# Kernel optimization log

Hardware: AMD Instinct MI355X
Metric: run time of the kernel (lower is better)

Reference implementation:

```python
import jax, jax.numpy as jnp
import numpy as np

G, C, L, D, H, NCLS = 64, 32, 128, 64, 128, 10


def setup_inputs() -> dict:
    key = jax.random.key(0)
    ks = jax.random.split(key, 5)
    scale = 0.05
    return {
        "cycle_reps": jax.random.normal(ks[0], (G, C, L, D), dtype=jnp.float32),
        "W_ih": jax.random.normal(ks[1], (4 * H, D), dtype=jnp.float32) * scale,
        "W_hh": jax.random.normal(ks[2], (4 * H, H), dtype=jnp.float32) * scale,
        "b_ih": jnp.zeros((4 * H,), dtype=jnp.float32),
        "b_hh": jnp.zeros((4 * H,), dtype=jnp.float32),
        "W_cls": jax.random.normal(ks[3], (NCLS, H), dtype=jnp.float32) * scale,
        "b_cls": jnp.zeros((NCLS,), dtype=jnp.float32),
    }


def _lstm_seq_sum(x, W_ih, W_hh, b):
    """Run a single-layer LSTM over x [B, L, D]; return sum of hidden states over L -> [B, H]."""
    B = x.shape[0]
    Hh = W_hh.shape[1]
    # precompute input-side gate pre-activations for all timesteps: [L, B, 4H]
    xg = jnp.einsum('bld,gd->lbg', x, W_ih) + b

    def step(carry, xg_t):
        h, c = carry
        gates = xg_t + h @ W_hh.T  # [B, 4H]
        i, f, g, o = jnp.split(gates, 4, axis=-1)  # torch i/f/g/o gate order
        i = jax.nn.sigmoid(i)
        f = jax.nn.sigmoid(f)
        g = jnp.tanh(g)
        o = jax.nn.sigmoid(o)
        c = f * c + i * g
        h = o * jnp.tanh(c)
        return (h, c), h

    init = (jnp.zeros((B, Hh), x.dtype), jnp.zeros((B, Hh), x.dtype))
    _, hs = jax.lax.scan(step, init, xg)  # hs: [L, B, H]
    return hs.sum(axis=0)


def reference(cycle_reps, W_ih, W_hh, b_ih, b_hh, W_cls, b_cls):
    Gn, Cn, Ln, Dn = cycle_reps.shape
    x = cycle_reps.reshape(Gn * Cn, Ln, Dn)
    rep = _lstm_seq_sum(x, W_ih, W_hh, b_ih + b_hh)  # [G*C, H]: sum of LSTM outputs over seq
    rep = rep.reshape(Gn, Cn, -1)
    # torch.var_mean over the cycle axis; only the mean is used as the graph rep
    graph_mean = rep.mean(axis=1)  # [G, H]
    logits = graph_mean @ W_cls.T + b_cls  # classifier_gnn
    return jax.nn.log_softmax(logits, axis=1)
```

## Files before the change

kernel.cpp:

```cpp
#include <hip/hip_runtime.h>
#include <hip/hip_bf16.h>

#define NSEQ 2048
#define LSEQ 128
#define DIN  64
#define HID  128
#define NCLS 10
#define XPAD 72
#define CHK  16

typedef __attribute__((ext_vector_type(8))) short bfrag8;
typedef __attribute__((ext_vector_type(4))) float facc4;

__device__ __forceinline__ short f2bf(float f) {
    union { __hip_bfloat16 b; short s; } u;
    u.b = __float2bfloat16(f);
    return u.s;
}

__device__ __forceinline__ bfrag8 load_bf16_frag(const float* __restrict__ p) {
    bfrag8 r;
#pragma unroll
    for (int j = 0; j < 8; ++j) r[j] = f2bf(p[j]);
    return r;
}

__device__ __forceinline__ float fast_sigmoid(float x) {
    float e = __builtin_amdgcn_exp2f(-1.4426950408889634f * x);
    return __builtin_amdgcn_rcpf(1.0f + e);
}
__device__ __forceinline__ float fast_tanh(float x) {
    float e = __builtin_amdgcn_exp2f(2.8853900817779268f * x);
    return 1.0f - 2.0f * __builtin_amdgcn_rcpf(1.0f + e);
}

__global__ __launch_bounds__(512) void lstm_fused(
    const float* __restrict__ x,
    const float* __restrict__ Wih,
    const float* __restrict__ Whh,
    const float* __restrict__ bih,
    const float* __restrict__ bhh,
    float* __restrict__ rep)
{
    __shared__ __align__(16) __hip_bfloat16 hbuf[2][16][136];
    __shared__ __align__(16) __hip_bfloat16 xs[2][CHK][8][XPAD];

    const int tid  = threadIdx.x;
    const int w    = tid >> 6;
    const int lane = tid & 63;
    const int ln   = lane & 15;
    const int qd   = lane >> 4;
    const int s0   = blockIdx.x * 8;
    const int khid = w * 16 + ln;
    const int sq0  = (qd & 1) * 4 + (qd >> 1) * 2;
    const int sq1  = sq0 + 1;
    const bool hi  = (qd >= 2);

    bfrag8 whh[4][4];
    bfrag8 wih[4][2];
    float  biasv[4];
#pragma unroll
    for (int g = 0; g < 4; ++g) {
        const int col = g * HID + khid;
        biasv[g] = bih[col] + bhh[col];
#pragma unroll
        for (int k0 = 0; k0 < 4; ++k0)
            whh[g][k0] = load_bf16_frag(Whh + col * HID + k0 * 32 + qd * 8);
#pragma unroll
        for (int k0 = 0; k0 < 2; ++k0)
            wih[g][k0] = load_bf16_frag(Wih + col * DIN + k0 * 32 + qd * 8);
    }

    {
        unsigned int* p = (unsigned int*)&hbuf[0][0][0];
        for (int i = tid; i < 2 * 16 * 136 / 2; i += 512) p[i] = 0u;
    }

    const float* xsrc = x + (size_t)(s0 + w) * (LSEQ * DIN) + lane * 16;
    const int stt = lane >> 2;
    const int sdd = (lane & 3) * 16;

    {
        float4 a0 = ((const float4*)xsrc)[0];
        float4 a1 = ((const float4*)xsrc)[1];
        float4 a2 = ((const float4*)xsrc)[2];
        float4 a3 = ((const float4*)xsrc)[3];
        bfrag8 o0, o1;
#pragma unroll
        for (int j = 0; j < 4; ++j) { o0[j] = f2bf(((float*)&a0)[j]); o0[4+j] = f2bf(((float*)&a1)[j]); }
#pragma unroll
        for (int j = 0; j < 4; ++j) { o1[j] = f2bf(((float*)&a2)[j]); o1[4+j] = f2bf(((float*)&a3)[j]); }
        *(bfrag8*)&xs[0][stt][w][sdd]     = o0;
        *(bfrag8*)&xs[0][stt][w][sdd + 8] = o1;
    }

    float cst[2]  = {0.f, 0.f};
    float hsum[2] = {0.f, 0.f};

    __syncthreads();

    facc4 accA[4], accB[4];
    {
        bfrag8 x0 = *(const bfrag8*)(&xs[0][0][ln & 7][qd * 8]);
        bfrag8 x1 = *(const bfrag8*)(&xs[0][0][ln & 7][32 + qd * 8]);
#pragma unroll
        for (int g = 0; g < 4; ++g) {
            accA[g] = (facc4){biasv[g], biasv[g], biasv[g], biasv[g]};
            accA[g] = __builtin_amdgcn_mfma_f32_16x16x32_bf16(x0, wih[g][0], accA[g], 0, 0, 0);
            accA[g] = __builtin_amdgcn_mfma_f32_16x16x32_bf16(x1, wih[g][1], accA[g], 0, 0, 0);
        }
    }

    int cur = 0;

#define STEP(ACCIN, ACCOUT, CT)                                                          \
    {                                                                                    \
        const int ct = (CT);                                                             \
                                             \
        bfrag8 hf[4];                                                                    \
        _Pragma("unroll")                                                                \
        for (int k0 = 0; k0 < 4; ++k0)                                                   \
            hf[k0] = *(const bfrag8*)(&hbuf[cur][ln][k0 * 32 + qd * 8]);                 \
             \
        const int nbuf = (ct < CHK - 1) ? buf : (buf ^ 1);                               \
        const int nct  = (ct + 1) & (CHK - 1);                                           \
        bfrag8 xf0 = *(const bfrag8*)(&xs[nbuf][nct][ln & 7][qd * 8]);                   \
        bfrag8 xf1 = *(const bfrag8*)(&xs[nbuf][nct][ln & 7][32 + qd * 8]);              \
                    \
        _Pragma("unroll")                                                                \
        for (int g = 0; g < 4; ++g)                                                      \
            _Pragma("unroll")                                                            \
            for (int k0 = 0; k0 < 4; ++k0)                                               \
                ACCIN[g] = __builtin_amdgcn_mfma_f32_16x16x32_bf16(hf[k0], whh[g][k0], ACCIN[g], 0, 0, 0); \
                \
        float rc2[4], rc3[4];                                                            \
        _Pragma("unroll")                                                                \
        for (int g = 0; g < 4; ++g) {                                                    \
            rc2[g] = __shfl_xor(ACCIN[g][2], 32);                                        \
            rc3[g] = __shfl_xor(ACCIN[g][3], 32);                                        \
        }                                                                                \
                              \
        _Pragma("unroll")                                                                \
        for (int g = 0; g < 4; ++g) {                                                    \
            ACCOUT[g] = (facc4){biasv[g], biasv[g], biasv[g], biasv[g]};                 \
            ACCOUT[g] = __builtin_amdgcn_mfma_f32_16x16x32_bf16(xf0, wih[g][0], ACCOUT[g], 0, 0, 0); \
            ACCOUT[g] = __builtin_amdgcn_mfma_f32_16x16x32_bf16(xf1, wih[g][1], ACCOUT[g], 0, 0, 0); \
        }                                                                                \
        if (ct == 0 && more) {                      \
            const float* p = xsrc + (chunk + 1) * (CHK * DIN);                           \
            l0 = ((const float4*)p)[0];                                                  \
            l1 = ((const float4*)p)[1];                                                  \
            l2 = ((const float4*)p)[2];                                                  \
            l3 = ((const float4*)p)[3];                                                  \
        }                                                                                \
        if (ct == 12 && more) {                   \
            bfrag8 o0, o1;                                                               \
            _Pragma("unroll")                                                            \
            for (int j = 0; j < 4; ++j) { o0[j] = f2bf(((float*)&l0)[j]); o0[4+j] = f2bf(((float*)&l1)[j]); } \
            _Pragma("unroll")                                                            \
            for (int j = 0; j < 4; ++j) { o1[j] = f2bf(((float*)&l2)[j]); o1[4+j] = f2bf(((float*)&l3)[j]); } \
            *(bfrag8*)&xs[buf ^ 1][stt][w][sdd]     = o0;                                \
            *(bfrag8*)&xs[buf ^ 1][stt][w][sdd + 8] = o1;                                \
        }                                                                                \
                               \
        short hb[2];                                                                     \
        _Pragma("unroll")                                                                \
        for (int j = 0; j < 2; ++j) {                                                    \
            float u0 = hi ? (j ? rc3[0] : rc2[0]) : ACCIN[0][j];                         \
            float u1 = hi ? (j ? rc3[1] : rc2[1]) : ACCIN[1][j];                         \
            float u2 = hi ? (j ? rc3[2] : rc2[2]) : ACCIN[2][j];                         \
            float u3 = hi ? (j ? rc3[3] : rc2[3]) : ACCIN[3][j];                         \
            float iv = fast_sigmoid(u0);                                                 \
            float fv = fast_sigmoid(u1);                                                 \
            float gv = fast_tanh(u2);                                                    \
            float ov = fast_sigmoid(u3);                                                 \
            float c  = fv * cst[j] + iv * gv;                                            \
            cst[j]   = c;                                                                \
            float hv = ov * fast_tanh(c);                                                \
            hsum[j] += hv;                                                               \
            hb[j]    = f2bf(hv);                                                         \
        }                                                                                \
        ((short*)&hbuf[cur ^ 1][sq0][0])[khid] = hb[0];                                  \
        ((short*)&hbuf[cur ^ 1][sq1][0])[khid] = hb[1];                                  \
        __syncthreads();                                                                 \
        cur ^= 1;                                                                        \
    }

    for (int chunk = 0; chunk < LSEQ / CHK; ++chunk) {
        const int buf = chunk & 1;
        const bool more = chunk < (LSEQ / CHK - 1);
        float4 l0, l1, l2, l3;
#pragma unroll 1
        for (int ct2 = 0; ct2 < CHK / 2; ++ct2) {
            STEP(accA, accB, 2 * ct2);
            STEP(accB, accA, 2 * ct2 + 1);
        }
    }
#undef STEP

    rep[(size_t)(s0 + sq0) * HID + khid] = hsum[0];
    rep[(size_t)(s0 + sq1) * HID + khid] = hsum[1];
}

__global__ __launch_bounds__(128) void cls_kernel(
    const float* __restrict__ rep,
    const float* __restrict__ Wcls,
    const float* __restrict__ bcls,
    float* __restrict__ out)
{
    __shared__ float m_s[HID];
    __shared__ float logits_s[NCLS];
    const int g = blockIdx.x;
    const int h = threadIdx.x;

    float s = 0.f;
#pragma unroll 4
    for (int c = 0; c < 32; ++c)
        s += rep[((size_t)g * 32 + c) * HID + h];
    m_s[h] = s * (1.0f / 32.0f);
    __syncthreads();

    if (h < NCLS) {
        float acc = bcls[h];
        for (int k = 0; k < HID; ++k)
            acc += m_s[k] * Wcls[h * HID + k];
        logits_s[h] = acc;
    }
    __syncthreads();

    if (h < NCLS) {
        float mx = logits_s[0];
#pragma unroll
        for (int j = 1; j < NCLS; ++j) mx = fmaxf(mx, logits_s[j]);
        float se = 0.f;
#pragma unroll
        for (int j = 0; j < NCLS; ++j)
            se += __builtin_amdgcn_exp2f((logits_s[j] - mx) * 1.4426950408889634f);
        float lse = mx + 0.6931471805599453f * __builtin_amdgcn_logf(se);
        out[g * NCLS + h] = logits_s[h] - lse;
    }
}

extern "C" void kernel_launch(void* const* d_in, const int* in_sizes, int n_in,
                              void* d_out, int out_size, void* d_ws, size_t ws_size,
                              hipStream_t stream) {
    const float* x    = (const float*)d_in[0];
    const float* Wih  = (const float*)d_in[1];
    const float* Whh  = (const float*)d_in[2];
    const float* bih  = (const float*)d_in[3];
    const float* bhh  = (const float*)d_in[4];
    const float* Wcls = (const float*)d_in[5];
    const float* bcls = (const float*)d_in[6];

    float* rep = (float*)d_ws;

    lstm_fused<<<NSEQ / 8, 512, 0, stream>>>(x, Wih, Whh, bih, bhh, rep);
    cls_kernel<<<64, 128, 0, stream>>>(rep, Wcls, bcls, (float*)d_out);
}
```

Measured before the change: 201.3 us.

## Fuse classifier into LSTM kernel via atomic ticket, switch to fp16 MFMA

The classifier kernel is removed. Each LSTM block atomically adds its per-graph hidden-state mean into a workspace buffer, and the last block, found through an atomic ticket counter, computes logits and log-softmax. Weights, inputs and hidden state switch from bf16 to fp16 MFMA, and the cross-half lane shuffle uses permlane32_swap where available. This saves one kernel launch and the rep round-trip, and it adds a memset, float atomics and a serialized tail in the last block.

```diff
diff --git a/kernel.cpp b/kernel.cpp
--- a/kernel.cpp
+++ b/kernel.cpp
@@ -9,19 +9,14 @@
 #define XPAD 72
 #define CHK  16
 
-typedef __attribute__((ext_vector_type(8))) short bfrag8;
-typedef __attribute__((ext_vector_type(4))) float facc4;
-
-__device__ __forceinline__ short f2bf(float f) {
-    union { __hip_bfloat16 b; short s; } u;
-    u.b = __float2bfloat16(f);
-    return u.s;
-}
-
-__device__ __forceinline__ bfrag8 load_bf16_frag(const float* __restrict__ p) {
-    bfrag8 r;
-#pragma unroll
-    for (int j = 0; j < 8; ++j) r[j] = f2bf(p[j]);
+typedef _Float16 f16x8 __attribute__((ext_vector_type(8)));
+typedef float    facc4 __attribute__((ext_vector_type(4)));
+typedef unsigned uint2v __attribute__((ext_vector_type(2)));
+
+__device__ __forceinline__ f16x8 load_f16_frag(const float* __restrict__ p) {
+    f16x8 r;
+#pragma unroll
+    for (int j = 0; j < 8; ++j) r[j] = (_Float16)p[j];
     return r;
 }
 
@@ -32,6 +27,17 @@
 __device__ __forceinline__ float fast_tanh(float x) {
     float e = __builtin_amdgcn_exp2f(2.8853900817779268f * x);
     return 1.0f - 2.0f * __builtin_amdgcn_rcpf(1.0f + e);
+}
+
+__device__ __forceinline__ float half_exchange(float a, float b, bool hi) {
+#if __has_builtin(__builtin_amdgcn_permlane32_swap)
+    uint2v r = __builtin_amdgcn_permlane32_swap(
+        __builtin_bit_cast(unsigned, a), __builtin_bit_cast(unsigned, b), false, false);
+    return __builtin_bit_cast(float, r.x);
+#else
+    float bx = __shfl_xor(b, 32);
+    return hi ? bx : a;
+#endif
 }
 
 __global__ __launch_bounds__(512) void lstm_fused(
@@ -40,10 +46,16 @@
     const float* __restrict__ Whh,
     const float* __restrict__ bih,
     const float* __restrict__ bhh,
-    float* __restrict__ rep)
+    const float* __restrict__ Wcls,
+    const float* __restrict__ bcls,
+    float* __restrict__ meanf,
+    unsigned* __restrict__ ticket,
+    float* __restrict__ out)
 {
-    __shared__ __align__(16) __hip_bfloat16 hbuf[2][16][136];
-    __shared__ __align__(16) __hip_bfloat16 xs[2][CHK][8][XPAD];
+    __shared__ __align__(16) _Float16 hbuf[2][16][136];
+    __shared__ __align__(16) _Float16 xs[2][CHK][8][XPAD];
+    __shared__ float logit_s[64 * NCLS];
+    __shared__ unsigned tick_s;
 
     const int tid  = threadIdx.x;
     const int w    = tid >> 6;
@@ -56,19 +68,20 @@
     const int sq1  = sq0 + 1;
     const bool hi  = (qd >= 2);
 
-    bfrag8 whh[4][4];
-    bfrag8 wih[4][2];
-    float  biasv[4];
+    f16x8 whh[4][4];
+    f16x8 wih[4][2];
+    facc4 biasf[4];
 #pragma unroll
     for (int g = 0; g < 4; ++g) {
         const int col = g * HID + khid;
-        biasv[g] = bih[col] + bhh[col];
+        float b = bih[col] + bhh[col];
+        biasf[g] = (facc4){b, b, b, b};
 #pragma unroll
         for (int k0 = 0; k0 < 4; ++k0)
-            whh[g][k0] = load_bf16_frag(Whh + col * HID + k0 * 32 + qd * 8);
+            whh[g][k0] = load_f16_frag(Whh + col * HID + k0 * 32 + qd * 8);
 #pragma unroll
         for (int k0 = 0; k0 < 2; ++k0)
-            wih[g][k0] = load_bf16_frag(Wih + col * DIN + k0 * 32 + qd * 8);
+            wih[g][k0] = load_f16_frag(Wih + col * DIN + k0 * 32 + qd * 8);
     }
 
     {
@@ -85,13 +98,13 @@
         float4 a1 = ((const float4*)xsrc)[1];
         float4 a2 = ((const float4*)xsrc)[2];
         float4 a3 = ((const float4*)xsrc)[3];
-        bfrag8 o0, o1;
-#pragma unroll
-        for (int j = 0; j < 4; ++j) { o0[j] = f2bf(((float*)&a0)[j]); o0[4+j] = f2bf(((float*)&a1)[j]); }
-#pragma unroll
-        for (int j = 0; j < 4; ++j) { o1[j] = f2bf(((float*)&a2)[j]); o1[4+j] = f2bf(((float*)&a3)[j]); }
-        *(bfrag8*)&xs[0][stt][w][sdd]     = o0;
-        *(bfrag8*)&xs[0][stt][w][sdd + 8] = o1;
+        f16x8 o0, o1;
+#pragma unroll
+        for (int j = 0; j < 4; ++j) { o0[j] = (_Float16)((float*)&a0)[j]; o0[4+j] = (_Float16)((float*)&a1)[j]; }
+#pragma unroll
+        for (int j = 0; j < 4; ++j) { o1[j] = (_Float16)((float*)&a2)[j]; o1[4+j] = (_Float16)((float*)&a3)[j]; }
+        *(f16x8*)&xs[0][stt][w][sdd]     = o0;
+        *(f16x8*)&xs[0][stt][w][sdd + 8] = o1;
     }
 
     float cst[2]  = {0.f, 0.f};
@@ -101,13 +114,12 @@
 
     facc4 accA[4], accB[4];
     {
-        bfrag8 x0 = *(const bfrag8*)(&xs[0][0][ln & 7][qd * 8]);
-        bfrag8 x1 = *(const bfrag8*)(&xs[0][0][ln & 7][32 + qd * 8]);
+        f16x8 x0 = *(const f16x8*)(&xs[0][0][ln & 7][qd * 8]);
+        f16x8 x1 = *(const f16x8*)(&xs[0][0][ln & 7][32 + qd * 8]);
 #pragma unroll
         for (int g = 0; g < 4; ++g) {
-            accA[g] = (facc4){biasv[g], biasv[g], biasv[g], biasv[g]};
-            accA[g] = __builtin_amdgcn_mfma_f32_16x16x32_bf16(x0, wih[g][0], accA[g], 0, 0, 0);
-            accA[g] = __builtin_amdgcn_mfma_f32_16x16x32_bf16(x1, wih[g][1], accA[g], 0, 0, 0);
+            accA[g] = __builtin_amdgcn_mfma_f32_16x16x32_f16(x0, wih[g][0], biasf[g], 0, 0, 0);
+            accA[g] = __builtin_amdgcn_mfma_f32_16x16x32_f16(x1, wih[g][1], accA[g], 0, 0, 0);
         }
     }
 
@@ -117,34 +129,33 @@
     {                                                                                    \
         const int ct = (CT);                                                             \
                                              \
-        bfrag8 hf[4];                                                                    \
+        f16x8 hf[4];                                                                     \
         _Pragma("unroll")                                                                \
         for (int k0 = 0; k0 < 4; ++k0)                                                   \
-            hf[k0] = *(const bfrag8*)(&hbuf[cur][ln][k0 * 32 + qd * 8]);                 \
-             \
+            hf[k0] = *(const f16x8*)(&hbuf[cur][ln][k0 * 32 + qd * 8]);                  \
+                                                                  \
         const int nbuf = (ct < CHK - 1) ? buf : (buf ^ 1);                               \
         const int nct  = (ct + 1) & (CHK - 1);                                           \
-        bfrag8 xf0 = *(const bfrag8*)(&xs[nbuf][nct][ln & 7][qd * 8]);                   \
-        bfrag8 xf1 = *(const bfrag8*)(&xs[nbuf][nct][ln & 7][32 + qd * 8]);              \
-                    \
+        f16x8 xf0 = *(const f16x8*)(&xs[nbuf][nct][ln & 7][qd * 8]);                     \
+        f16x8 xf1 = *(const f16x8*)(&xs[nbuf][nct][ln & 7][32 + qd * 8]);                \
+                          \
         _Pragma("unroll")                                                                \
         for (int g = 0; g < 4; ++g)                                                      \
             _Pragma("unroll")                                                            \
             for (int k0 = 0; k0 < 4; ++k0)                                               \
-                ACCIN[g] = __builtin_amdgcn_mfma_f32_16x16x32_bf16(hf[k0], whh[g][k0], ACCIN[g], 0, 0, 0); \
-                \
-        float rc2[4], rc3[4];                                                            \
+                ACCIN[g] = __builtin_amdgcn_mfma_f32_16x16x32_f16(hf[k0], whh[g][k0], ACCIN[g], 0, 0, 0); \
+                    \
+        float u0[4], u1[4];                                                              \
         _Pragma("unroll")                                                                \
         for (int g = 0; g < 4; ++g) {                                                    \
-            rc2[g] = __shfl_xor(ACCIN[g][2], 32);                                        \
-            rc3[g] = __shfl_xor(ACCIN[g][3], 32);                                        \
+            u0[g] = half_exchange(ACCIN[g][0], ACCIN[g][2], hi);                         \
+            u1[g] = half_exchange(ACCIN[g][1], ACCIN[g][3], hi);                         \
         }                                                                                \
                               \
         _Pragma("unroll")                                                                \
         for (int g = 0; g < 4; ++g) {                                                    \
-            ACCOUT[g] = (facc4){biasv[g], biasv[g], biasv[g], biasv[g]};                 \
-            ACCOUT[g] = __builtin_amdgcn_mfma_f32_16x16x32_bf16(xf0, wih[g][0], ACCOUT[g], 0, 0, 0); \
-            ACCOUT[g] = __builtin_amdgcn_mfma_f32_16x16x32_bf16(xf1, wih[g][1], ACCOUT[g], 0, 0, 0); \
+            ACCOUT[g] = __builtin_amdgcn_mfma_f32_16x16x32_f16(xf0, wih[g][0], biasf[g], 0, 0, 0); \
+            ACCOUT[g] = __builtin_amdgcn_mfma_f32_16x16x32_f16(xf1, wih[g][1], ACCOUT[g], 0, 0, 0); \
         }                                                                                \
         if (ct == 0 && more) {                      \
             const float* p = xsrc + (chunk + 1) * (CHK * DIN);                           \
@@ -154,34 +165,34 @@
             l3 = ((const float4*)p)[3];                                                  \
         }                                                                                \
         if (ct == 12 && more) {                   \
-            bfrag8 o0, o1;                                                               \
+            f16x8 o0, o1;                                                                \
             _Pragma("unroll")                                                            \
-            for (int j = 0; j < 4; ++j) { o0[j] = f2bf(((float*)&l0)[j]); o0[4+j] = f2bf(((float*)&l1)[j]); } \
+            for (int j = 0; j < 4; ++j) { o0[j] = (_Float16)((float*)&l0)[j]; o0[4+j] = (_Float16)((float*)&l1)[j]; } \
             _Pragma("unroll")                                                            \
-            for (int j = 0; j < 4; ++j) { o1[j] = f2bf(((float*)&l2)[j]); o1[4+j] = f2bf(((float*)&l3)[j]); } \
-            *(bfrag8*)&xs[buf ^ 1][stt][w][sdd]     = o0;                                \
-            *(bfrag8*)&xs[buf ^ 1][stt][w][sdd + 8] = o1;                                \
+            for (int j = 0; j < 4; ++j) { o1[j] = (_Float16)((float*)&l2)[j]; o1[4+j] = (_Float16)((float*)&l3)[j]; } \
+            *(f16x8*)&xs[buf ^ 1][stt][w][sdd]     = o0;                                 \
+            *(f16x8*)&xs[buf ^ 1][stt][w][sdd + 8] = o1;                                 \
         }                                                                                \
                                \
-        short hb[2];                                                                     \
+        _Float16 hb[2];                                                                  \
         _Pragma("unroll")                                                                \
         for (int j = 0; j < 2; ++j) {                                                    \
-            float u0 = hi ? (j ? rc3[0] : rc2[0]) : ACCIN[0][j];                         \
-            float u1 = hi ? (j ? rc3[1] : rc2[1]) : ACCIN[1][j];                         \
-            float u2 = hi ? (j ? rc3[2] : rc2[2]) : ACCIN[2][j];                         \
-            float u3 = hi ? (j ? rc3[3] : rc2[3]) : ACCIN[3][j];                         \
-            float iv = fast_sigmoid(u0);                                                 \
-            float fv = fast_sigmoid(u1);                                                 \
-            float gv = fast_tanh(u2);                                                    \
-            float ov = fast_sigmoid(u3);                                                 \
+            float g0v = j ? u1[0] : u0[0];                                               \
+            float g1v = j ? u1[1] : u0[1];                                               \
+            float g2v = j ? u1[2] : u0[2];                                               \
+            float g3v = j ? u1[3] : u0[3];                                               \
+            float iv = fast_sigmoid(g0v);                                                \
+            float fv = fast_sigmoid(g1v);                                                \
+            float gv = fast_tanh(g2v);                                                   \
+            float ov = fast_sigmoid(g3v);                                                \
             float c  = fv * cst[j] + iv * gv;                                            \
             cst[j]   = c;                                                                \
             float hv = ov * fast_tanh(c);                                                \
             hsum[j] += hv;                                                               \
-            hb[j]    = f2bf(hv);                                                         \
-        }                                                                                \
-        ((short*)&hbuf[cur ^ 1][sq0][0])[khid] = hb[0];                                  \
-        ((short*)&hbuf[cur ^ 1][sq1][0])[khid] = hb[1];                                  \
+            hb[j]    = (_Float16)hv;                                                     \
+        }                                                                                \
+        hbuf[cur ^ 1][sq0][khid] = hb[0];                                                \
+        hbuf[cur ^ 1][sq1][khid] = hb[1];                                                \
         __syncthreads();                                                                 \
         cur ^= 1;                                                                        \
     }
@@ -198,46 +209,40 @@
     }
 #undef STEP
 
-    rep[(size_t)(s0 + sq0) * HID + khid] = hsum[0];
-    rep[(size_t)(s0 + sq1) * HID + khid] = hsum[1];
-}
-
-__global__ __launch_bounds__(128) void cls_kernel(
-    const float* __restrict__ rep,
-    const float* __restrict__ Wcls,
-    const float* __restrict__ bcls,
-    float* __restrict__ out)
-{
-    __shared__ float m_s[HID];
-    __shared__ float logits_s[NCLS];
-    const int g = blockIdx.x;
-    const int h = threadIdx.x;
-
-    float s = 0.f;
-#pragma unroll 4
-    for (int c = 0; c < 32; ++c)
-        s += rep[((size_t)g * 32 + c) * HID + h];
-    m_s[h] = s * (1.0f / 32.0f);
+    atomicAdd(meanf + (s0 >> 5) * HID + khid, (hsum[0] + hsum[1]) * (1.0f / 32.0f));
+
+    __threadfence();
     __syncthreads();
-
-    if (h < NCLS) {
-        float acc = bcls[h];
-        for (int k = 0; k < HID; ++k)
-            acc += m_s[k] * Wcls[h * HID + k];
-        logits_s[h] = acc;
-    }
+    if (tid == 0) tick_s = atomicAdd(ticket, 1u);
     __syncthreads();
-
-    if (h < NCLS) {
-        float mx = logits_s[0];
-#pragma unroll
-        for (int j = 1; j < NCLS; ++j) mx = fmaxf(mx, logits_s[j]);
-        float se = 0.f;
-#pragma unroll
-        for (int j = 0; j < NCLS; ++j)
-            se += __builtin_amdgcn_exp2f((logits_s[j] - mx) * 1.4426950408889634f);
-        float lse = mx + 0.6931471805599453f * __builtin_amdgcn_logf(se);
-        out[g * NCLS + h] = logits_s[h] - lse;
+    if (tick_s == 255u) {
+        __threadfence();
+        for (int d = tid; d < 64 * NCLS; d += 512) {
+            const int g  = d / NCLS;
+            const int cl = d - g * NCLS;
+            float acc = bcls[cl];
+            const float* mrow = meanf + g * HID;
+            const float* wrow = Wcls + cl * HID;
+#pragma unroll 8
+            for (int k = 0; k < HID; ++k)
+                acc += mrow[k] * wrow[k];
+            logit_s[d] = acc;
+        }
+        __syncthreads();
+        if (tid < 64) {
+            const float* lg = logit_s + tid * NCLS;
+            float mx = lg[0];
+#pragma unroll
+            for (int j = 1; j < NCLS; ++j) mx = fmaxf(mx, lg[j]);
+            float se = 0.f;
+#pragma unroll
+            for (int j = 0; j < NCLS; ++j)
+                se += __builtin_amdgcn_exp2f((lg[j] - mx) * 1.4426950408889634f);
+            float lse = mx + 0.6931471805599453f * __builtin_amdgcn_logf(se);
+#pragma unroll
+            for (int j = 0; j < NCLS; ++j)
+                out[tid * NCLS + j] = lg[j] - lse;
+        }
     }
 }
 
@@ -252,8 +257,12 @@
     const float* Wcls = (const float*)d_in[5];
     const float* bcls = (const float*)d_in[6];
 
-    float* rep = (float*)d_ws;
-
-    lstm_fused<<<NSEQ / 8, 512, 0, stream>>>(x, Wih, Whh, bih, bhh, rep);
-    cls_kernel<<<64, 128, 0, stream>>>(rep, Wcls, bcls, (float*)d_out);
-}
+    float*    meanf  = (float*)d_ws;
+    unsigned* ticket = (unsigned*)((char*)d_ws + 64 * HID * 4);
+
+    hipMemsetAsync(d_ws, 0, 64 * HID * 4 + 64, stream);
+
+    lstm_fused<<<NSEQ / 8, 512, 0, stream>>>(x, Wih, Whh, bih, bhh,
+                                             Wcls, bcls, meanf, ticket,
+                                             (float*)d_out);
+}
```

Result: slower. 236.9 us (+17.7%).
